# Optimization experiments

Measured on AMD Instinct MI355X. Metric: run time of the kernel, lower is better.

The kernel has to match this reference:

```python
import jax, jax.numpy as jnp
import numpy as np

B = 4096
INPUT_SIZE = 256
OUT_WINDOW = 10
C = 16
OUTPUT_SIZE = 2  # real/imag pair
WIN = INPUT_SIZE - OUT_WINDOW + 1  # 247
BN_EPS = 1e-5


def setup_inputs() -> dict:
    key = jax.random.key(0)
    ks = jax.random.split(key, 7)
    return {
        "x": jax.random.normal(ks[0], (B, INPUT_SIZE, C, 2), dtype=jnp.float32),
        "W_in_real": jax.random.normal(ks[1], (C, WIN), dtype=jnp.float32),
        "W_in_imag": jax.random.normal(ks[2], (C, WIN), dtype=jnp.float32),
        "W_nl": jax.random.normal(ks[3], (C, OUTPUT_SIZE, 2 * (C - 1)), dtype=jnp.float32) * 0.1,
        "W_coeff": jax.random.normal(ks[4], (OUTPUT_SIZE, OUTPUT_SIZE), dtype=jnp.float32),
        "W_out_real": jax.random.normal(ks[5], (C, OUT_WINDOW), dtype=jnp.float32),
        "W_out_imag": jax.random.normal(ks[6], (C, OUT_WINDOW), dtype=jnp.float32),
        "bn_gamma": jnp.ones((C,), jnp.float32),
        "bn_beta": jnp.zeros((C,), jnp.float32),
    }


def _depthwise_filter(x_bcn, w_ck):
    # per-channel valid cross-correlation: out[b,c,w] = sum_k x[b,c,w+k] * w_ck[c,k]
    kern = w_ck[:, None, :]  # (O=C, I/groups=1, K)
    return jax.lax.conv_general_dilated(
        x_bcn, kern, window_strides=(1,), padding="VALID",
        dimension_numbers=("NCH", "OIH", "NCH"), feature_group_count=C)


def reference(x, W_in_real, W_in_imag, W_nl, W_coeff, W_out_real, W_out_imag, bn_gamma, bn_beta):
    # x: [B, N, C, 2]
    x_real = jnp.transpose(x[..., 0], (0, 2, 1))  # [B, C, N]
    x_imag = jnp.transpose(x[..., 1], (0, 2, 1))
    # unfold + per-channel FIR filter == depthwise valid correlation -> [B, W, C]
    f_r = jnp.transpose(_depthwise_filter(x_real, W_in_real), (0, 2, 1))
    f_i = jnp.transpose(_depthwise_filter(x_imag, W_in_imag), (0, 2, 1))
    # cubic amplitude nonlinearity
    amp = f_r * f_r + f_i * f_i
    f_r = amp * f_r
    f_i = amp * f_i
    # masked cross-channel gather (all channels except self), static indices
    nbr = np.stack([np.delete(np.arange(C), c) for c in range(C)])  # [C, C-1]
    nonlin_in = jnp.concatenate([f_r[:, :, nbr], f_i[:, :, nbr]], axis=-1)  # [B, W, C, 2(C-1)]
    # per-channel mixing then shared coeff mix
    nonlin_out = jnp.einsum("bwcf,cof->bwco", nonlin_in, W_nl)   # [B, W, C, 2]
    coeff_out = jnp.einsum("bwco,po->bwcp", nonlin_out, W_coeff)  # [B, W, C, 2]
    # per-channel output FIR over the out_window axis
    out_r = jnp.einsum("bwc,cw->bc", coeff_out[..., 0], W_out_real)
    out_i = jnp.einsum("bwc,cw->bc", coeff_out[..., 1], W_out_imag)
    out = jnp.stack([out_r, out_i], axis=-1)  # [B, C, 2]
    # BatchNorm1d over channel axis C (training mode, biased batch stats)
    mu = jnp.mean(out, axis=(0, 2))
    var = jnp.mean(jnp.square(out - mu[None, :, None]), axis=(0, 2))
    scale = (bn_gamma * jax.lax.rsqrt(var + BN_EPS))[None, :, None]
    return (out - mu[None, :, None]) * scale + bn_beta[None, :, None]
```

## Files before the change

kernel.cpp:

```cpp
#include <hip/hip_runtime.h>

#define BTOT 4096
#define G 4
#define NC 16
#define WIN 247
#define NBLK (BTOT / G)

#define F2IDX(m, c) ((m) * 16 + (c) + ((m) >> 6) * 8)
#define WTSZ 4272

__global__ __launch_bounds__(256, 4) void k_main(
    const float* __restrict__ x,
    const float* __restrict__ Wr, const float* __restrict__ Wi,
    const float* __restrict__ Wnl, const float* __restrict__ Wc,
    const float* __restrict__ Wor, const float* __restrict__ Woi,
    float* __restrict__ out, float* __restrict__ ws)
{
    __shared__ float2 WT[WTSZ];
    __shared__ float Mlds[4 * 16 * 17];
    __shared__ float WoS[2 * 160];
    __shared__ float WcS[4];

    const int tid  = threadIdx.x;
    const int lane = tid & 63;
    const int wv   = tid >> 6;
    const int ns   = lane >> 4;
    const int c    = lane & 15;
    const int n0   = ns * 64;
    const int b0   = blockIdx.x * G;

    for (int idx = tid; idx < 265 * 16; idx += 256) {
        int m = idx >> 4, cc = idx & 15;
        int t = m - 9;
        float2 v = make_float2(0.f, 0.f);
        if (t >= 0 && t < WIN) { v.x = Wr[cc * WIN + t]; v.y = Wi[cc * WIN + t]; }
        WT[F2IDX(m, cc)] = v;
    }
    for (int idx = tid; idx < 1024; idx += 256) {
        int m  = idx >> 8;
        int cc = (idx >> 4) & 15;
        int j  = idx & 15;
        float v = 0.f;
        if (j != cc) {
            int jj = j - (j > cc);
            v = Wnl[cc * 60 + (m >> 1) * 30 + (m & 1) * 15 + jj];
        }
        Mlds[m * 272 + cc * 17 + j] = v;
    }
    if (tid < 160) { WoS[tid] = Wor[tid]; WoS[160 + tid] = Woi[tid]; }
    if (tid < 4) WcS[tid] = Wc[tid];
    __syncthreads();

    const float2* xp = (const float2*)x + (size_t)(b0 + wv) * 4096 + c;

    float accr[10], acci[10];
    float2 win[11];
    float2 xr[16];
    #pragma unroll
    for (int w = 0; w < 10; ++w) { accr[w] = 0.f; acci[w] = 0.f; }

    #pragma unroll
    for (int j = 0; j < 11; ++j) win[j] = WT[F2IDX(n0 + j, c)];
    #pragma unroll
    for (int j = 0; j < 16; ++j) xr[j] = xp[(n0 + j) * 16];

    #pragma unroll
    for (int i = 0; i < 64; ++i) {
        float2 xv = xr[i & 15];
        if (i < 48) xr[i & 15] = xp[(n0 + i + 16) * 16];
        #pragma unroll
        for (int w = 0; w < 10; ++w) {
            float2 wt = win[(i + 9 - w) % 11];
            accr[w] = fmaf(xv.x, wt.x, accr[w]);
            acci[w] = fmaf(xv.y, wt.y, acci[w]);
        }
        if (i < 62) win[i % 11] = WT[F2IDX(n0 + 11 + i, c)];
    }

    #pragma unroll
    for (int w = 0; w < 10; ++w) {
        accr[w] += __shfl_xor(accr[w], 16);  accr[w] += __shfl_xor(accr[w], 32);
        acci[w] += __shfl_xor(acci[w], 16);  acci[w] += __shfl_xor(acci[w], 32);
    }

    __syncthreads();
    float* S    = (float*)WT;
    float* fbuf = S;
    float* crS  = S + 1280;
    float* ciS  = S + 1920;
    float* red  = S + 2560;
    float* redq = S + 2624;

    if (lane < 16) {
        #pragma unroll
        for (int w = 0; w < 10; ++w) {
            float fr = accr[w], fi = acci[w];
            float a  = fr * fr + fi * fi;
            fbuf[wv * 320 + c * 20 + w]      = a * fr;
            fbuf[wv * 320 + c * 20 + 10 + w] = a * fi;
        }
    }
    __syncthreads();

    const float* M0r = Mlds;
    const float* M0i = Mlds + 272;
    const float* M1r = Mlds + 544;
    const float* M1i = Mlds + 816;
    for (int idx = tid; idx < G * 160; idx += 256) {
        int bb = idx / 160; int r = idx - bb * 160;
        int cc = r / 10;    int w = r - cc * 10;
        const float* f3 = fbuf + bb * 320;
        float s0 = 0.f, s1 = 0.f;
        #pragma unroll
        for (int j = 0; j < NC; ++j) {
            float f3r = f3[j * 20 + w];
            float f3i = f3[j * 20 + 10 + w];
            s0 = fmaf(f3r, M0r[cc * 17 + j], fmaf(f3i, M0i[cc * 17 + j], s0));
            s1 = fmaf(f3r, M1r[cc * 17 + j], fmaf(f3i, M1i[cc * 17 + j], s1));
        }
        float p0 = s0 * WcS[0] + s1 * WcS[1];
        float p1 = s0 * WcS[2] + s1 * WcS[3];
        crS[idx] = p0 * WoS[cc * 10 + w];
        ciS[idx] = p1 * WoS[160 + cc * 10 + w];
    }
    __syncthreads();

    if (tid < G * NC) {
        int bb = tid >> 4; int cc = tid & 15;
        float orr = 0.f, oii = 0.f;
        #pragma unroll
        for (int w = 0; w < 10; ++w) {
            orr += crS[bb * 160 + cc * 10 + w];
            oii += ciS[bb * 160 + cc * 10 + w];
        }
        size_t o = ((size_t)(b0 + bb) * NC + cc) * 2;
        out[o]     = orr;
        out[o + 1] = oii;
        red[tid]  = orr + oii;
        redq[tid] = orr * orr + oii * oii;
    }
    __syncthreads();
    if (tid < NC) {
        float s = 0.f, qq = 0.f;
        #pragma unroll
        for (int bb = 0; bb < G; ++bb) { s += red[bb * 16 + tid]; qq += redq[bb * 16 + tid]; }
        ws[(tid * NBLK + blockIdx.x) * 2]     = s;
        ws[(tid * NBLK + blockIdx.x) * 2 + 1] = qq;
    }
}

__global__ __launch_bounds__(256) void k_bnstat(
    const float* __restrict__ ws_in, float* __restrict__ ws_ab,
    const float* __restrict__ gamma, const float* __restrict__ beta)
{
    const int cch = blockIdx.x;
    const int tid = threadIdx.x;
    float s = 0.f, q = 0.f;
    for (int i = tid; i < NBLK; i += 256) {
        s += ws_in[(cch * NBLK + i) * 2];
        q += ws_in[(cch * NBLK + i) * 2 + 1];
    }
    #pragma unroll
    for (int off = 32; off; off >>= 1) {
        s += __shfl_down(s, off, 64);
        q += __shfl_down(q, off, 64);
    }
    __shared__ float rs[4], rq[4];
    const int wv = tid >> 6;
    if ((tid & 63) == 0) { rs[wv] = s; rq[wv] = q; }
    __syncthreads();
    if (tid == 0) {
        s = rs[0] + rs[1] + rs[2] + rs[3];
        q = rq[0] + rq[1] + rq[2] + rq[3];
        const float inv_n = 1.f / (BTOT * 2.f);
        float mu  = s * inv_n;
        float var = q * inv_n - mu * mu;
        float sc  = gamma[cch] * rsqrtf(var + 1e-5f);
        ws_ab[cch]      = sc;
        ws_ab[16 + cch] = beta[cch] - mu * sc;
    }
}

__global__ __launch_bounds__(256) void k_bnapply(
    float* __restrict__ out, const float* __restrict__ ws_ab)
{
    __shared__ float A[16], Bb[16];
    const int tid = threadIdx.x;
    if (tid < 16) { A[tid] = ws_ab[tid]; Bb[tid] = ws_ab[16 + tid]; }
    __syncthreads();
    int j = blockIdx.x * 256 + tid;
    if (j < BTOT * NC) {
        float2* o2 = (float2*)out + j;
        int cch = j & 15;
        float2 v = *o2;
        v.x = v.x * A[cch] + Bb[cch];
        v.y = v.y * A[cch] + Bb[cch];
        *o2 = v;
    }
}

extern "C" void kernel_launch(void* const* d_in, const int* in_sizes, int n_in,
                              void* d_out, int out_size, void* d_ws, size_t ws_size,
                              hipStream_t stream)
{
    const float* x    = (const float*)d_in[0];
    const float* Wr   = (const float*)d_in[1];
    const float* Wi   = (const float*)d_in[2];
    const float* Wnl  = (const float*)d_in[3];
    const float* Wc   = (const float*)d_in[4];
    const float* Wor  = (const float*)d_in[5];
    const float* Woi  = (const float*)d_in[6];
    const float* gam  = (const float*)d_in[7];
    const float* bet  = (const float*)d_in[8];
    float* out = (float*)d_out;
    float* ws  = (float*)d_ws;
    float* ws_ab = ws + NC * NBLK * 2;

    k_main<<<NBLK, 256, 0, stream>>>(x, Wr, Wi, Wnl, Wc, Wor, Woi, out, ws);
    k_bnstat<<<NC, 256, 0, stream>>>(ws, ws_ab, gam, bet);
    k_bnapply<<<(BTOT * NC + 255) / 256, 256, 0, stream>>>(out, ws_ab);
}
```

Before: 52.06 us.

## Fuse BN stat and apply kernels, vectorize FIR with packed FMA

The main kernel now writes per-sample partial sums straight to the workspace instead of reducing them per block. The separate stat and apply kernels are merged into one kernel in which every block redundantly reduces all 4096 partials per channel before normalizing its slice. The FIR inner loop uses 2-wide vector FMAs, which can map to packed FP32 instructions, and the x prefetch depth drops from 16 to 8. This removes one launch and one block-level reduction, but each of the 256 BN blocks now rereads the full 512 KB of partials.

```diff
diff --git a/kernel.cpp b/kernel.cpp
--- a/kernel.cpp
+++ b/kernel.cpp
@@ -5,6 +5,8 @@
 #define NC 16
 #define WIN 247
 #define NBLK (BTOT / G)
+
+typedef float v2f __attribute__((ext_vector_type(2)));
 
 #define F2IDX(m, c) ((m) * 16 + (c) + ((m) >> 6) * 8)
 #define WTSZ 4272
@@ -16,7 +18,7 @@
     const float* __restrict__ Wor, const float* __restrict__ Woi,
     float* __restrict__ out, float* __restrict__ ws)
 {
-    __shared__ float2 WT[WTSZ];
+    __shared__ v2f WT[WTSZ];
     __shared__ float Mlds[4 * 16 * 17];
     __shared__ float WoS[2 * 160];
     __shared__ float WcS[4];
@@ -32,7 +34,7 @@
     for (int idx = tid; idx < 265 * 16; idx += 256) {
         int m = idx >> 4, cc = idx & 15;
         int t = m - 9;
-        float2 v = make_float2(0.f, 0.f);
+        v2f v = (v2f)(0.f);
         if (t >= 0 && t < WIN) { v.x = Wr[cc * WIN + t]; v.y = Wi[cc * WIN + t]; }
         WT[F2IDX(m, cc)] = v;
     }
@@ -51,36 +53,35 @@
     if (tid < 4) WcS[tid] = Wc[tid];
     __syncthreads();
 
-    const float2* xp = (const float2*)x + (size_t)(b0 + wv) * 4096 + c;
-
-    float accr[10], acci[10];
-    float2 win[11];
-    float2 xr[16];
-    #pragma unroll
-    for (int w = 0; w < 10; ++w) { accr[w] = 0.f; acci[w] = 0.f; }
+    const v2f* xp = (const v2f*)x + (size_t)(b0 + wv) * 4096 + c;
+
+    v2f acc[10];
+    v2f win[11];
+    v2f xr[8];
+    #pragma unroll
+    for (int w = 0; w < 10; ++w) acc[w] = (v2f)(0.f);
 
     #pragma unroll
     for (int j = 0; j < 11; ++j) win[j] = WT[F2IDX(n0 + j, c)];
     #pragma unroll
-    for (int j = 0; j < 16; ++j) xr[j] = xp[(n0 + j) * 16];
+    for (int j = 0; j < 8; ++j) xr[j] = xp[(n0 + j) * 16];
 
     #pragma unroll
     for (int i = 0; i < 64; ++i) {
-        float2 xv = xr[i & 15];
-        if (i < 48) xr[i & 15] = xp[(n0 + i + 16) * 16];
+        v2f xv = xr[i & 7];
+        if (i < 56) xr[i & 7] = xp[(n0 + i + 8) * 16];
         #pragma unroll
         for (int w = 0; w < 10; ++w) {
-            float2 wt = win[(i + 9 - w) % 11];
-            accr[w] = fmaf(xv.x, wt.x, accr[w]);
-            acci[w] = fmaf(xv.y, wt.y, acci[w]);
+            v2f wt = win[(i + 9 - w) % 11];
+            acc[w] = __builtin_elementwise_fma(xv, wt, acc[w]);
         }
         if (i < 62) win[i % 11] = WT[F2IDX(n0 + 11 + i, c)];
     }
 
     #pragma unroll
     for (int w = 0; w < 10; ++w) {
-        accr[w] += __shfl_xor(accr[w], 16);  accr[w] += __shfl_xor(accr[w], 32);
-        acci[w] += __shfl_xor(acci[w], 16);  acci[w] += __shfl_xor(acci[w], 32);
+        acc[w].x += __shfl_xor(acc[w].x, 16);  acc[w].x += __shfl_xor(acc[w].x, 32);
+        acc[w].y += __shfl_xor(acc[w].y, 16);  acc[w].y += __shfl_xor(acc[w].y, 32);
     }
 
     __syncthreads();
@@ -88,13 +89,11 @@
     float* fbuf = S;
     float* crS  = S + 1280;
     float* ciS  = S + 1920;
-    float* red  = S + 2560;
-    float* redq = S + 2624;
 
     if (lane < 16) {
         #pragma unroll
         for (int w = 0; w < 10; ++w) {
-            float fr = accr[w], fi = acci[w];
+            float fr = acc[w].x, fi = acc[w].y;
             float a  = fr * fr + fi * fi;
             fbuf[wv * 320 + c * 20 + w]      = a * fr;
             fbuf[wv * 320 + c * 20 + 10 + w] = a * fi;
@@ -136,67 +135,49 @@
         size_t o = ((size_t)(b0 + bb) * NC + cc) * 2;
         out[o]     = orr;
         out[o + 1] = oii;
-        red[tid]  = orr + oii;
-        redq[tid] = orr * orr + oii * oii;
-    }
-    __syncthreads();
-    if (tid < NC) {
-        float s = 0.f, qq = 0.f;
-        #pragma unroll
-        for (int bb = 0; bb < G; ++bb) { s += red[bb * 16 + tid]; qq += redq[bb * 16 + tid]; }
-        ws[(tid * NBLK + blockIdx.x) * 2]     = s;
-        ws[(tid * NBLK + blockIdx.x) * 2 + 1] = qq;
+        float2* p2 = (float2*)ws;
+        p2[cc * BTOT + b0 + bb] =
+            make_float2(orr + oii, orr * orr + oii * oii);
     }
 }
 
-__global__ __launch_bounds__(256) void k_bnstat(
-    const float* __restrict__ ws_in, float* __restrict__ ws_ab,
-    const float* __restrict__ gamma, const float* __restrict__ beta)
+__global__ __launch_bounds__(256) void k_bn(
+    const float* __restrict__ ws_in,
+    const float* __restrict__ gamma, const float* __restrict__ beta,
+    float* __restrict__ out)
 {
-    const int cch = blockIdx.x;
+    __shared__ float A[16], Bb[16];
     const int tid = threadIdx.x;
+    const int cch = tid >> 4;
+    const int t   = tid & 15;
+    const float2* p2 = (const float2*)ws_in;
     float s = 0.f, q = 0.f;
-    for (int i = tid; i < NBLK; i += 256) {
-        s += ws_in[(cch * NBLK + i) * 2];
-        q += ws_in[(cch * NBLK + i) * 2 + 1];
-    }
-    #pragma unroll
-    for (int off = 32; off; off >>= 1) {
-        s += __shfl_down(s, off, 64);
-        q += __shfl_down(q, off, 64);
-    }
-    __shared__ float rs[4], rq[4];
-    const int wv = tid >> 6;
-    if ((tid & 63) == 0) { rs[wv] = s; rq[wv] = q; }
-    __syncthreads();
-    if (tid == 0) {
-        s = rs[0] + rs[1] + rs[2] + rs[3];
-        q = rq[0] + rq[1] + rq[2] + rq[3];
+    #pragma unroll 4
+    for (int k = 0; k < BTOT / 16; ++k) {
+        float2 v = p2[cch * BTOT + t + 16 * k];
+        s += v.x; q += v.y;
+    }
+    #pragma unroll
+    for (int off = 1; off < 16; off <<= 1) {
+        s += __shfl_xor(s, off);
+        q += __shfl_xor(q, off);
+    }
+    if (t == 0) {
         const float inv_n = 1.f / (BTOT * 2.f);
         float mu  = s * inv_n;
         float var = q * inv_n - mu * mu;
         float sc  = gamma[cch] * rsqrtf(var + 1e-5f);
-        ws_ab[cch]      = sc;
-        ws_ab[16 + cch] = beta[cch] - mu * sc;
-    }
-}
-
-__global__ __launch_bounds__(256) void k_bnapply(
-    float* __restrict__ out, const float* __restrict__ ws_ab)
-{
-    __shared__ float A[16], Bb[16];
-    const int tid = threadIdx.x;
-    if (tid < 16) { A[tid] = ws_ab[tid]; Bb[tid] = ws_ab[16 + tid]; }
+        A[cch]  = sc;
+        Bb[cch] = beta[cch] - mu * sc;
+    }
     __syncthreads();
     int j = blockIdx.x * 256 + tid;
-    if (j < BTOT * NC) {
-        float2* o2 = (float2*)out + j;
-        int cch = j & 15;
-        float2 v = *o2;
-        v.x = v.x * A[cch] + Bb[cch];
-        v.y = v.y * A[cch] + Bb[cch];
-        *o2 = v;
-    }
+    float2* o2 = (float2*)out + j;
+    int c2 = j & 15;
+    float2 v = *o2;
+    v.x = v.x * A[c2] + Bb[c2];
+    v.y = v.y * A[c2] + Bb[c2];
+    *o2 = v;
 }
 
 extern "C" void kernel_launch(void* const* d_in, const int* in_sizes, int n_in,
@@ -214,9 +195,7 @@
     const float* bet  = (const float*)d_in[8];
     float* out = (float*)d_out;
     float* ws  = (float*)d_ws;
-    float* ws_ab = ws + NC * NBLK * 2;
 
     k_main<<<NBLK, 256, 0, stream>>>(x, Wr, Wi, Wnl, Wc, Wor, Woi, out, ws);
-    k_bnstat<<<NC, 256, 0, stream>>>(ws, ws_ab, gam, bet);
-    k_bnapply<<<(BTOT * NC + 255) / 256, 256, 0, stream>>>(out, ws_ab);
+    k_bn<<<BTOT * NC / 256, 256, 0, stream>>>(ws, gam, bet, out);
 }
```

After: 59.99 us. 15.2% more time.
